# Kernel tuning notes

Hardware: AMD Instinct MI355X
Metric: run time of the kernel (lower is better)

## Reference

```python
import jax, jax.numpy as jnp
import numpy as np

N_NODES = 100000
N_EDGES = 1600000
HIDDEN = 128
STEPS = 4
N_GRAPHS = 64


def setup_inputs() -> dict:
    key = jax.random.key(0)
    ks = jax.random.split(key, 8)
    x = jax.random.normal(ks[0], (N_NODES, HIDDEN), dtype=jnp.float32)
    edge_index = jax.random.randint(ks[1], (2, N_EDGES), 0, N_NODES, dtype=jnp.int64)
    batch = jnp.sort(jax.random.randint(ks[2], (N_NODES,), 0, N_GRAPHS, dtype=jnp.int64))
    s = 1.0 / np.sqrt(HIDDEN)
    weight = jax.random.normal(ks[3], (STEPS, HIDDEN, HIDDEN), dtype=jnp.float32) * s
    w_ih = jax.random.normal(ks[4], (3 * HIDDEN, HIDDEN), dtype=jnp.float32) * s
    w_hh = jax.random.normal(ks[5], (3 * HIDDEN, HIDDEN), dtype=jnp.float32) * s
    b_ih = jnp.zeros((3 * HIDDEN,), dtype=jnp.float32)
    b_hh = jnp.zeros((3 * HIDDEN,), dtype=jnp.float32)
    return {"x": x, "edge_index": edge_index, "batch": batch,
            "weight": weight, "w_ih": w_ih, "w_hh": w_hh,
            "b_ih": b_ih, "b_hh": b_hh}


def _gru_cell(m, h, w_ih, w_hh, b_ih, b_hh):
    # PyTorch GRUCell: gates ordered (r, z, n)
    gi = m @ w_ih.T + b_ih  # [N, 3H]
    gh = h @ w_hh.T + b_hh  # [N, 3H]
    i_r, i_z, i_n = jnp.split(gi, 3, axis=-1)
    h_r, h_z, h_n = jnp.split(gh, 3, axis=-1)
    r = jax.nn.sigmoid(i_r + h_r)
    z = jax.nn.sigmoid(i_z + h_z)
    n = jnp.tanh(i_n + r * h_n)
    return (1.0 - z) * n + z * h


def reference(x, edge_index, batch, weight, w_ih, w_hh, b_ih, b_hh):
    src, dst = edge_index[0], edge_index[1]
    h = x
    for i in range(STEPS):
        m = h @ weight[i]  # [N, H]
        # message = m[src] scattered (add) into dst
        aggr = jax.ops.segment_sum(m[src], dst, num_segments=N_NODES)
        h = _gru_cell(aggr, h, w_ih, w_hh, b_ih, b_hh)
    h = jax.nn.relu(h)
    # global mean pool per graph
    sums = jax.ops.segment_sum(h, batch, num_segments=N_GRAPHS)  # [G, H]
    counts = jax.ops.segment_sum(jnp.ones((N_NODES,), h.dtype), batch, num_segments=N_GRAPHS)
    return sums / jnp.maximum(counts, 1.0)[:, None]
```

## Files before the change

kernel.cpp:

```cpp
#include <hip/hip_runtime.h>

#define N_NODES  100000
#define N_EDGES  1600000
#define HIDDEN   128
#define STEPS    4
#define N_GRAPHS 64
#define NBUCK    256
#define BWID     391
#define OUT_P    136

typedef unsigned short u16;
typedef unsigned int   u32;
typedef unsigned long long u64;
typedef __attribute__((ext_vector_type(8))) short bf16x8;
typedef __attribute__((ext_vector_type(4))) float f32x4;

__device__ inline u16 f2bf(float f) {
  u32 u = __float_as_uint(f);
  u = (u + 0x7FFFu + ((u >> 16) & 1u)) >> 16;
  return (u16)u;
}
__device__ inline float bf2f(u16 b) { return __uint_as_float(((u32)b) << 16); }

__device__ inline float fast_sig(float x) { return 1.f / (1.f + __expf(-x)); }
__device__ inline float fast_tanh(float x) {
  x = fminf(fmaxf(x, -15.f), 15.f);
  float e = __expf(2.f * x);
  return (e - 1.f) / (e + 1.f);
}

__global__ __launch_bounds__(1024) void k_bhist(const int* __restrict__ edst,
                                                int* __restrict__ bcnt) {
  __shared__ int hist[NBUCK];
  int tid = threadIdx.x;
  if (tid < NBUCK) hist[tid] = 0;
  __syncthreads();
  int e0 = blockIdx.x * 4096;
  #pragma unroll
  for (int i = 0; i < 4; ++i) {
    int e = e0 + i * 1024 + tid;
    if (e < N_EDGES) atomicAdd(&hist[(u32)edst[e] / (u32)BWID], 1);
  }
  __syncthreads();
  if (tid < NBUCK) atomicAdd(&bcnt[tid], hist[tid]);
}

__global__ void k_bscan(const int* __restrict__ bcnt, int* __restrict__ ebase,
                        int* __restrict__ gcursor) {
  __shared__ int buf[NBUCK];
  int t = threadIdx.x;
  int v = bcnt[t];
  buf[t] = v;
  __syncthreads();
  for (int off = 1; off < NBUCK; off <<= 1) {
    int u = 0;
    if (t >= off) u = buf[t - off];
    __syncthreads();
    buf[t] += u;
    __syncthreads();
  }
  int ex = buf[t] - v;
  ebase[t] = ex;
  gcursor[t] = ex;
  if (t == NBUCK - 1) ebase[NBUCK] = buf[t];
}

__global__ __launch_bounds__(1024) void k_part(const int* __restrict__ esrc,
                                               const int* __restrict__ edst,
                                               int* __restrict__ gcursor,
                                               u64* __restrict__ ebuf) {
  __shared__ int hist[NBUCK];
  __shared__ int base[NBUCK];
  int tid = threadIdx.x;
  if (tid < NBUCK) hist[tid] = 0;
  __syncthreads();
  int e0 = blockIdx.x * 4096;
  int sv[4], dv[4], bk[4], rk[4];
  #pragma unroll
  for (int i = 0; i < 4; ++i) {
    int e = e0 + i * 1024 + tid;
    if (e < N_EDGES) {
      sv[i] = esrc[e];
      dv[i] = edst[e];
      bk[i] = (int)((u32)dv[i] / (u32)BWID);
      rk[i] = atomicAdd(&hist[bk[i]], 1);
    } else bk[i] = -1;
  }
  __syncthreads();
  if (tid < NBUCK) base[tid] = atomicAdd(&gcursor[tid], hist[tid]);
  __syncthreads();
  #pragma unroll
  for (int i = 0; i < 4; ++i) {
    if (bk[i] >= 0) {
      int pos = base[bk[i]] + rk[i];
      ebuf[pos] = ((u64)(u32)dv[i] << 32) | (u32)sv[i];
    }
  }
}

__global__ __launch_bounds__(1024) void k_csr(const u64* __restrict__ ebuf,
                                              const int* __restrict__ ebase,
                                              int* __restrict__ offs,
                                              int* __restrict__ csr) {
  __shared__ int lcnt[512];
  __shared__ int lofs[512];
  int b = blockIdx.x, tid = threadIdx.x;
  int n0 = b * BWID;
  int n1 = min(n0 + BWID, N_NODES);
  int nn = n1 - n0;
  int e0 = ebase[b], e1 = ebase[b + 1];
  if (tid < 512) lcnt[tid] = 0;
  __syncthreads();
  for (int e = e0 + tid; e < e1; e += 1024) {
    int dst = (int)(ebuf[e] >> 32);
    atomicAdd(&lcnt[dst - n0], 1);
  }
  __syncthreads();
  if (tid < 512) lofs[tid] = lcnt[tid];
  __syncthreads();
  for (int off = 1; off < 512; off <<= 1) {
    int v = 0;
    if (tid < 512 && tid >= off) v = lofs[tid - off];
    __syncthreads();
    if (tid < 512 && tid >= off) lofs[tid] += v;
    __syncthreads();
  }
  int nodeoff = 0;
  if (tid < 512) nodeoff = e0 + lofs[tid] - lcnt[tid];
  if (tid < 512) lofs[tid] = nodeoff;
  if (tid < nn) offs[n0 + tid] = nodeoff;
  if (b == 0 && tid == 0) offs[N_NODES] = N_EDGES;
  __syncthreads();
  for (int e = e0 + tid; e < e1; e += 1024) {
    u64 p = ebuf[e];
    int src = (int)(p & 0xffffffffull);
    int dst = (int)(p >> 32);
    int pos = atomicAdd(&lofs[dst - n0], 1);
    csr[pos] = src;
  }
}

__global__ void k_wb(const float* __restrict__ W, const float* __restrict__ w_ih,
                     const float* __restrict__ w_hh, u16* __restrict__ bsw) {
  __shared__ float wrow[128];
  int b = blockIdx.x, st = b >> 8, k = b & 255, t = threadIdx.x;
  if (k < 128) wrow[t] = W[(st * 128 + k) * 128 + t];
  __syncthreads();
  int kc = k >> 5, quad = (k >> 3) & 3, kl = k & 7;
  u16* base = bsw + (size_t)st * 131072 + kc * 16384;
  #pragma unroll
  for (int gq = 0; gq < 4; ++gq) {
    int c = gq * 128 + t;
    float v;
    if (k < 128) {
      if (c < 384) {
        const float* wr = w_ih + c * 128;
        float sacc = 0.f;
        for (int j = 0; j < 128; ++j) sacc += wrow[j] * wr[j];
        v = sacc;
      } else v = 0.f;
    } else {
      int kk = k - 128;
      if (c < 256)      v = w_hh[c * 128 + kk];
      else if (c < 384) v = 0.f;
      else              v = w_hh[(c - 128) * 128 + kk];
    }
    int gi = c >> 7, cw = c & 127;
    int wv = cw >> 5, hu = (cw >> 4) & 1, nl = c & 15;
    int slot = wv * 8 + gi * 2 + hu;
    base[(slot * 4 + quad) * 128 + nl * 8 + kl] = f2bf(v);
  }
}

__global__ void k_convert(const float* __restrict__ x, u16* __restrict__ h) {
  int i = (blockIdx.x * 256 + threadIdx.x) * 4;
  float4 v = *(const float4*)(x + i);
  u16 o[4] = {f2bf(v.x), f2bf(v.y), f2bf(v.z), f2bf(v.w)};
  *(uint2*)(h + i) = *(uint2*)o;
}

__global__ void k_gather(const u16* __restrict__ h, const int* __restrict__ csr,
                         const int* __restrict__ offs, u16* __restrict__ s) {
  int node = blockIdx.x * 4 + (threadIdx.x >> 6);
  int lane = threadIdx.x & 63;
  int q   = lane >> 4;
  int sub = lane & 15;
  int beg = offs[node], end = offs[node + 1];
  float a0 = 0.f, a1 = 0.f, a2 = 0.f, a3 = 0.f;
  float a4 = 0.f, a5 = 0.f, a6 = 0.f, a7 = 0.f;
  for (int j = beg + q; j < end; j += 4) {
    int src = csr[j];
    uint4 p = *(const uint4*)(h + (size_t)src * 128 + sub * 8);
    a0 += bf2f((u16)(p.x & 0xffffu)); a1 += bf2f((u16)(p.x >> 16));
    a2 += bf2f((u16)(p.y & 0xffffu)); a3 += bf2f((u16)(p.y >> 16));
    a4 += bf2f((u16)(p.z & 0xffffu)); a5 += bf2f((u16)(p.z >> 16));
    a6 += bf2f((u16)(p.w & 0xffffu)); a7 += bf2f((u16)(p.w >> 16));
  }
  a0 += __shfl_xor(a0, 16); a0 += __shfl_xor(a0, 32);
  a1 += __shfl_xor(a1, 16); a1 += __shfl_xor(a1, 32);
  a2 += __shfl_xor(a2, 16); a2 += __shfl_xor(a2, 32);
  a3 += __shfl_xor(a3, 16); a3 += __shfl_xor(a3, 32);
  a4 += __shfl_xor(a4, 16); a4 += __shfl_xor(a4, 32);
  a5 += __shfl_xor(a5, 16); a5 += __shfl_xor(a5, 32);
  a6 += __shfl_xor(a6, 16); a6 += __shfl_xor(a6, 32);
  a7 += __shfl_xor(a7, 16); a7 += __shfl_xor(a7, 32);
  if (q == 0) {
    uint4 o;
    o.x = (u32)f2bf(a0) | ((u32)f2bf(a1) << 16);
    o.y = (u32)f2bf(a2) | ((u32)f2bf(a3) << 16);
    o.z = (u32)f2bf(a4) | ((u32)f2bf(a5) << 16);
    o.w = (u32)f2bf(a6) | ((u32)f2bf(a7) << 16);
    *(uint4*)(s + (size_t)node * 128 + sub * 8) = o;
  }
}

__global__ __launch_bounds__(256, 3) void k_gemm_gru(
    const u16* __restrict__ s_mat, const u16* __restrict__ h_mat,
    const u16* __restrict__ bsw, const float* __restrict__ b_ih,
    const float* __restrict__ b_hh, u16* __restrict__ h_out) {
  __shared__ u16 Asw[8192];
  __shared__ u16 Osw[32 * OUT_P];

  const int tid  = threadIdx.x;
  const int wave = tid >> 6;
  const int lane = tid & 63;
  const int nl   = lane & 15;
  const int quad = lane >> 4;
  const int row0 = blockIdx.x * 32;

  {
    int snl = tid & 15, squad = (tid >> 4) & 3, sel = tid >> 6;
    int g = sel & 1, half = sel >> 1;
    const u16* row = (half ? h_mat : s_mat) + (size_t)(row0 + g * 16 + snl) * 128;
    #pragma unroll
    for (int kc2 = 0; kc2 < 4; ++kc2) {
      uint4 v = *(const uint4*)(row + kc2 * 32 + squad * 8);
      *(uint4*)&Asw[(((g * 8 + half * 4 + kc2) * 4 + squad) * 16 + snl) * 8] = v;
    }
  }
  __syncthreads();

  const u16* bp = bsw + wave * 8 * 512 + lane * 8;

  f32x4 acc[2][8];
  #pragma unroll
  for (int g = 0; g < 2; ++g)
    #pragma unroll
    for (int u = 0; u < 8; ++u) acc[g][u] = (f32x4){0.f, 0.f, 0.f, 0.f};

  bf16x8 bcur[6], bnext[6];
  #pragma unroll
  for (int i = 0; i < 6; ++i) bcur[i] = *(const bf16x8*)(bp + i * 512);

  #pragma unroll
  for (int kc = 0; kc < 8; ++kc) {
    if (kc < 7) {
      #pragma unroll
      for (int i = 0; i < 6; ++i) {
        int us = (kc + 1 < 4) ? i : (i < 4 ? i : i + 2);
        bnext[i] = *(const bf16x8*)(bp + (kc + 1) * 16384 + us * 512);
      }
    }
    bf16x8 a0 = *(const bf16x8*)&Asw[kc * 512 + lane * 8];
    bf16x8 a1 = *(const bf16x8*)&Asw[(8 + kc) * 512 + lane * 8];
    #pragma unroll
    for (int i = 0; i < 6; ++i) {
      int u = (kc < 4) ? i : (i < 4 ? i : i + 2);
      acc[0][u] = __builtin_amdgcn_mfma_f32_16x16x32_bf16(a0, bcur[i], acc[0][u], 0, 0, 0);
      acc[1][u] = __builtin_amdgcn_mfma_f32_16x16x32_bf16(a1, bcur[i], acc[1][u], 0, 0, 0);
    }
    #pragma unroll
    for (int i = 0; i < 6; ++i) bcur[i] = bnext[i];
  }

  float bias[8];
  #pragma unroll
  for (int u = 0; u < 8; ++u) {
    int gi = u >> 1, hu = u & 1;
    int cw = wave * 32 + hu * 16 + nl;
    bias[u] = (gi == 0) ? b_ih[cw] + b_hh[cw]
            : (gi == 1) ? b_ih[128 + cw] + b_hh[128 + cw]
            : (gi == 2) ? b_ih[256 + cw]
                        : b_hh[256 + cw];
  }

  #pragma unroll
  for (int g = 0; g < 2; ++g) {
    #pragma unroll
    for (int hu = 0; hu < 2; ++hu) {
      int cw = wave * 32 + hu * 16 + nl;
      int hbase = ((g * 8 + 4 + wave) * 4 + ((hu * 2 + (nl >> 3)) & 3)) * 128 + (nl & 7);
      #pragma unroll
      for (int i = 0; i < 4; ++i) {
        int m = quad * 4 + i;
        float rv = fast_sig(acc[g][0 + hu][i] + bias[0 + hu]);
        float zv = fast_sig(acc[g][2 + hu][i] + bias[2 + hu]);
        float iv = acc[g][4 + hu][i] + bias[4 + hu];
        float hn = acc[g][6 + hu][i] + bias[6 + hu];
        float hv = bf2f(Asw[hbase + m * 8]);
        float n  = fast_tanh(iv + rv * hn);
        float o  = (1.f - zv) * n + zv * hv;
        Osw[(g * 16 + m) * OUT_P + cw] = f2bf(o);
      }
    }
  }
  __syncthreads();

  {
    int r32 = tid >> 3, c0 = (tid & 7) * 16;
    uint4 v0 = *(const uint4*)&Osw[r32 * OUT_P + c0];
    uint4 v1 = *(const uint4*)&Osw[r32 * OUT_P + c0 + 8];
    uint4* dstp = (uint4*)(h_out + (size_t)(row0 + r32) * 128 + c0);
    dstp[0] = v0;
    dstp[1] = v1;
  }
}

__global__ void k_pool_partial(const u16* __restrict__ h, const int* __restrict__ batch,
                               float* __restrict__ acc) {
  int t = threadIdx.x;
  int node0 = blockIdx.x * 125;
  int node1 = node0 + 125;
  int cur = batch[node0];
  float sum = 0.f;
  for (int r = node0; r < node1; ++r) {
    int g = batch[r];
    if (g != cur) {
      atomicAdd(&acc[cur * 128 + t], sum);
      sum = 0.f;
      cur = g;
    }
    sum += fmaxf(bf2f(h[(size_t)r * 128 + t]), 0.f);
  }
  atomicAdd(&acc[cur * 128 + t], sum);
}

__global__ void k_pool_div(const float* __restrict__ acc, const int* __restrict__ batch,
                           float* __restrict__ out) {
  __shared__ int se[2];
  int g = blockIdx.x, t = threadIdx.x;
  if (t < 2) {
    int target = g + t;
    int lo = 0, hi = N_NODES;
    while (lo < hi) { int mid = (lo + hi) >> 1; if (batch[mid] < target) lo = mid + 1; else hi = mid; }
    se[t] = lo;
  }
  __syncthreads();
  int cnt = se[1] - se[0];
  out[g * 128 + t] = acc[g * 128 + t] / (float)(cnt > 0 ? cnt : 1);
}

extern "C" void kernel_launch(void* const* d_in, const int* in_sizes, int n_in,
                              void* d_out, int out_size, void* d_ws, size_t ws_size,
                              hipStream_t stream) {
  const float* x     = (const float*)d_in[0];
  const int*   edges = (const int*)d_in[1];
  const int*   batch = (const int*)d_in[2];
  const float* W     = (const float*)d_in[3];
  const float* w_ih  = (const float*)d_in[4];
  const float* w_hh  = (const float*)d_in[5];
  const float* b_ih  = (const float*)d_in[6];
  const float* b_hh  = (const float*)d_in[7];
  float* out = (float*)d_out;

  char* w = (char*)d_ws;
  u16* buf0    = (u16*)(w);
  u16* buf1    = (u16*)(w + 25600000);
  u16* bsw     = (u16*)(w + 51200000);
  float* acc   = (float*)(w + 52300032);
  int* offs    = (int*)(w + 52710400);
  int* gcursor = (int*)(w + 53120768);
  int* bcnt    = (int*)(w + 53122048);
  int* ebase   = (int*)(w + 53123328);
  int* csr     = (int*)(w + 53531136);
  u64* ebuf    = (u64*)buf1;

  const int* esrc = edges;
  const int* edst = edges + N_EDGES;

  hipMemsetAsync(bcnt, 0, NBUCK * sizeof(int), stream);
  k_bhist<<<391, 1024, 0, stream>>>(edst, bcnt);
  k_bscan<<<1, NBUCK, 0, stream>>>(bcnt, ebase, gcursor);
  k_part<<<391, 1024, 0, stream>>>(esrc, edst, gcursor, ebuf);
  k_csr<<<NBUCK, 1024, 0, stream>>>(ebuf, ebase, offs, csr);
  k_wb<<<1024, 128, 0, stream>>>(W, w_ih, w_hh, bsw);
  k_convert<<<(N_NODES * HIDDEN) / 1024, 256, 0, stream>>>(x, buf0);
  hipMemsetAsync(acc, 0, N_GRAPHS * HIDDEN * sizeof(float), stream);

  u16* hcur = buf0;
  u16* hnxt = buf1;
  for (int st = 0; st < STEPS; ++st) {
    k_gather<<<N_NODES / 4, 256, 0, stream>>>(hcur, csr, offs, hnxt);
    k_gemm_gru<<<N_NODES / 32, 256, 0, stream>>>(hnxt, hcur, bsw + st * 131072,
                                                 b_ih, b_hh, hnxt);
    u16* tmp = hcur; hcur = hnxt; hnxt = tmp;
  }
  k_pool_partial<<<800, 128, 0, stream>>>(hcur, batch, acc);
  k_pool_div<<<N_GRAPHS, 128, 0, stream>>>(acc, batch, out);
}
```

Before: 665.1 us.

## Drop edge histogram pass via fixed-capacity buckets and restructure neighbor gather

Edge partitioning now writes into fixed-capacity per-bucket slots, so the separate histogram kernel and memset are removed and the prefix scan runs after partitioning. The neighbor gather is restructured so each wave handles one node with every lane reading a 4-byte slice of each neighbor row, with eight neighbors unrolled to raise memory-level parallelism. The fixed bucket capacity assumes roughly uniform destination distribution and would overflow on skewed graphs.

```diff
diff --git a/kernel.cpp b/kernel.cpp
--- a/kernel.cpp
+++ b/kernel.cpp
@@ -7,6 +7,7 @@
 #define N_GRAPHS 64
 #define NBUCK    256
 #define BWID     391
+#define BCAP     7168
 #define OUT_P    136
 
 typedef unsigned short u16;
@@ -27,42 +28,6 @@
   x = fminf(fmaxf(x, -15.f), 15.f);
   float e = __expf(2.f * x);
   return (e - 1.f) / (e + 1.f);
-}
-
-__global__ __launch_bounds__(1024) void k_bhist(const int* __restrict__ edst,
-                                                int* __restrict__ bcnt) {
-  __shared__ int hist[NBUCK];
-  int tid = threadIdx.x;
-  if (tid < NBUCK) hist[tid] = 0;
-  __syncthreads();
-  int e0 = blockIdx.x * 4096;
-  #pragma unroll
-  for (int i = 0; i < 4; ++i) {
-    int e = e0 + i * 1024 + tid;
-    if (e < N_EDGES) atomicAdd(&hist[(u32)edst[e] / (u32)BWID], 1);
-  }
-  __syncthreads();
-  if (tid < NBUCK) atomicAdd(&bcnt[tid], hist[tid]);
-}
-
-__global__ void k_bscan(const int* __restrict__ bcnt, int* __restrict__ ebase,
-                        int* __restrict__ gcursor) {
-  __shared__ int buf[NBUCK];
-  int t = threadIdx.x;
-  int v = bcnt[t];
-  buf[t] = v;
-  __syncthreads();
-  for (int off = 1; off < NBUCK; off <<= 1) {
-    int u = 0;
-    if (t >= off) u = buf[t - off];
-    __syncthreads();
-    buf[t] += u;
-    __syncthreads();
-  }
-  int ex = buf[t] - v;
-  ebase[t] = ex;
-  gcursor[t] = ex;
-  if (t == NBUCK - 1) ebase[NBUCK] = buf[t];
 }
 
 __global__ __launch_bounds__(1024) void k_part(const int* __restrict__ esrc,
@@ -92,10 +57,27 @@
   #pragma unroll
   for (int i = 0; i < 4; ++i) {
     if (bk[i] >= 0) {
-      int pos = base[bk[i]] + rk[i];
+      int pos = bk[i] * BCAP + base[bk[i]] + rk[i];
       ebuf[pos] = ((u64)(u32)dv[i] << 32) | (u32)sv[i];
     }
   }
+}
+
+__global__ void k_bscan(const int* __restrict__ gcursor, int* __restrict__ ebase) {
+  __shared__ int buf[NBUCK];
+  int t = threadIdx.x;
+  int v = gcursor[t];
+  buf[t] = v;
+  __syncthreads();
+  for (int off = 1; off < NBUCK; off <<= 1) {
+    int u = 0;
+    if (t >= off) u = buf[t - off];
+    __syncthreads();
+    buf[t] += u;
+    __syncthreads();
+  }
+  ebase[t] = buf[t] - v;
+  if (t == NBUCK - 1) ebase[NBUCK] = buf[t];
 }
 
 __global__ __launch_bounds__(1024) void k_csr(const u64* __restrict__ ebuf,
@@ -108,11 +90,13 @@
   int n0 = b * BWID;
   int n1 = min(n0 + BWID, N_NODES);
   int nn = n1 - n0;
-  int e0 = ebase[b], e1 = ebase[b + 1];
+  int e0 = ebase[b];
+  int cnt = ebase[b + 1] - e0;
+  const u64* ebase_p = ebuf + (size_t)b * BCAP;
   if (tid < 512) lcnt[tid] = 0;
   __syncthreads();
-  for (int e = e0 + tid; e < e1; e += 1024) {
-    int dst = (int)(ebuf[e] >> 32);
+  for (int e = tid; e < cnt; e += 1024) {
+    int dst = (int)(ebase_p[e] >> 32);
     atomicAdd(&lcnt[dst - n0], 1);
   }
   __syncthreads();
@@ -131,8 +115,8 @@
   if (tid < nn) offs[n0 + tid] = nodeoff;
   if (b == 0 && tid == 0) offs[N_NODES] = N_EDGES;
   __syncthreads();
-  for (int e = e0 + tid; e < e1; e += 1024) {
-    u64 p = ebuf[e];
+  for (int e = tid; e < cnt; e += 1024) {
+    u64 p = ebase_p[e];
     int src = (int)(p & 0xffffffffull);
     int dst = (int)(p >> 32);
     int pos = atomicAdd(&lofs[dst - n0], 1);
@@ -183,35 +167,37 @@
                          const int* __restrict__ offs, u16* __restrict__ s) {
   int node = blockIdx.x * 4 + (threadIdx.x >> 6);
   int lane = threadIdx.x & 63;
-  int q   = lane >> 4;
-  int sub = lane & 15;
   int beg = offs[node], end = offs[node + 1];
-  float a0 = 0.f, a1 = 0.f, a2 = 0.f, a3 = 0.f;
-  float a4 = 0.f, a5 = 0.f, a6 = 0.f, a7 = 0.f;
-  for (int j = beg + q; j < end; j += 4) {
-    int src = csr[j];
-    uint4 p = *(const uint4*)(h + (size_t)src * 128 + sub * 8);
-    a0 += bf2f((u16)(p.x & 0xffffu)); a1 += bf2f((u16)(p.x >> 16));
-    a2 += bf2f((u16)(p.y & 0xffffu)); a3 += bf2f((u16)(p.y >> 16));
-    a4 += bf2f((u16)(p.z & 0xffffu)); a5 += bf2f((u16)(p.z >> 16));
-    a6 += bf2f((u16)(p.w & 0xffffu)); a7 += bf2f((u16)(p.w >> 16));
-  }
-  a0 += __shfl_xor(a0, 16); a0 += __shfl_xor(a0, 32);
-  a1 += __shfl_xor(a1, 16); a1 += __shfl_xor(a1, 32);
-  a2 += __shfl_xor(a2, 16); a2 += __shfl_xor(a2, 32);
-  a3 += __shfl_xor(a3, 16); a3 += __shfl_xor(a3, 32);
-  a4 += __shfl_xor(a4, 16); a4 += __shfl_xor(a4, 32);
-  a5 += __shfl_xor(a5, 16); a5 += __shfl_xor(a5, 32);
-  a6 += __shfl_xor(a6, 16); a6 += __shfl_xor(a6, 32);
-  a7 += __shfl_xor(a7, 16); a7 += __shfl_xor(a7, 32);
-  if (q == 0) {
-    uint4 o;
-    o.x = (u32)f2bf(a0) | ((u32)f2bf(a1) << 16);
-    o.y = (u32)f2bf(a2) | ((u32)f2bf(a3) << 16);
-    o.z = (u32)f2bf(a4) | ((u32)f2bf(a5) << 16);
-    o.w = (u32)f2bf(a6) | ((u32)f2bf(a7) << 16);
-    *(uint4*)(s + (size_t)node * 128 + sub * 8) = o;
-  }
+  float a0 = 0.f, a1 = 0.f;
+  int j = beg;
+  for (; j + 8 <= end; j += 8) {
+    int i0 = csr[j],     i1 = csr[j + 1], i2 = csr[j + 2], i3 = csr[j + 3];
+    int i4 = csr[j + 4], i5 = csr[j + 5], i6 = csr[j + 6], i7 = csr[j + 7];
+    u32 v0 = *(const u32*)(h + (size_t)i0 * 128 + lane * 2);
+    u32 v1 = *(const u32*)(h + (size_t)i1 * 128 + lane * 2);
+    u32 v2 = *(const u32*)(h + (size_t)i2 * 128 + lane * 2);
+    u32 v3 = *(const u32*)(h + (size_t)i3 * 128 + lane * 2);
+    u32 v4 = *(const u32*)(h + (size_t)i4 * 128 + lane * 2);
+    u32 v5 = *(const u32*)(h + (size_t)i5 * 128 + lane * 2);
+    u32 v6 = *(const u32*)(h + (size_t)i6 * 128 + lane * 2);
+    u32 v7 = *(const u32*)(h + (size_t)i7 * 128 + lane * 2);
+    a0 += __uint_as_float(v0 << 16); a1 += __uint_as_float(v0 & 0xffff0000u);
+    a0 += __uint_as_float(v1 << 16); a1 += __uint_as_float(v1 & 0xffff0000u);
+    a0 += __uint_as_float(v2 << 16); a1 += __uint_as_float(v2 & 0xffff0000u);
+    a0 += __uint_as_float(v3 << 16); a1 += __uint_as_float(v3 & 0xffff0000u);
+    a0 += __uint_as_float(v4 << 16); a1 += __uint_as_float(v4 & 0xffff0000u);
+    a0 += __uint_as_float(v5 << 16); a1 += __uint_as_float(v5 & 0xffff0000u);
+    a0 += __uint_as_float(v6 << 16); a1 += __uint_as_float(v6 & 0xffff0000u);
+    a0 += __uint_as_float(v7 << 16); a1 += __uint_as_float(v7 & 0xffff0000u);
+  }
+  for (; j < end; ++j) {
+    int i0 = csr[j];
+    u32 v0 = *(const u32*)(h + (size_t)i0 * 128 + lane * 2);
+    a0 += __uint_as_float(v0 << 16);
+    a1 += __uint_as_float(v0 & 0xffff0000u);
+  }
+  u32 o = (u32)f2bf(a0) | ((u32)f2bf(a1) << 16);
+  *(u32*)(s + (size_t)node * 128 + lane * 2) = o;
 }
 
 __global__ __launch_bounds__(256, 3) void k_gemm_gru(
@@ -370,7 +356,6 @@
   float* acc   = (float*)(w + 52300032);
   int* offs    = (int*)(w + 52710400);
   int* gcursor = (int*)(w + 53120768);
-  int* bcnt    = (int*)(w + 53122048);
   int* ebase   = (int*)(w + 53123328);
   int* csr     = (int*)(w + 53531136);
   u64* ebuf    = (u64*)buf1;
@@ -378,10 +363,9 @@
   const int* esrc = edges;
   const int* edst = edges + N_EDGES;
 
-  hipMemsetAsync(bcnt, 0, NBUCK * sizeof(int), stream);
-  k_bhist<<<391, 1024, 0, stream>>>(edst, bcnt);
-  k_bscan<<<1, NBUCK, 0, stream>>>(bcnt, ebase, gcursor);
+  hipMemsetAsync(gcursor, 0, NBUCK * sizeof(int), stream);
   k_part<<<391, 1024, 0, stream>>>(esrc, edst, gcursor, ebuf);
+  k_bscan<<<1, NBUCK, 0, stream>>>(gcursor, ebase);
   k_csr<<<NBUCK, 1024, 0, stream>>>(ebuf, ebase, offs, csr);
   k_wb<<<1024, 128, 0, stream>>>(W, w_ih, w_hh, bsw);
   k_convert<<<(N_NODES * HIDDEN) / 1024, 256, 0, stream>>>(x, buf0);
```

New measurement: 674.8 us. Within noise of the previous version (+1.4%).
